# Optimization experiments

Measured on AMD Instinct MI355X. Metric: run time of the kernel, lower is better.

## Reference

```python
import jax, jax.numpy as jnp
import numpy as np

N, C, E, H = 100000, 128, 640000, 128


def setup_inputs() -> dict:
    key = jax.random.key(0)
    ks = jax.random.split(key, 8)
    x = jax.random.normal(ks[0], (N, C), dtype=jnp.float32)
    # edges guaranteed to have no self-loops (module removes them then re-adds clean self-loops)
    rol = jax.random.randint(ks[1], (E,), 0, N, dtype=jnp.int32)
    off = jax.random.randint(ks[2], (E,), 1, N, dtype=jnp.int32)
    col = (rol + off) % N
    edge_index = jnp.stack([rol, col])  # [2, E]
    s = 1.0 / np.sqrt(C)
    return {
        "x": x,
        "edge_index": edge_index,
        "W_emb": jax.random.normal(ks[3], (C, C), dtype=jnp.float32) * s,
        "b_emb": jnp.zeros((C,), dtype=jnp.float32),
        "Wa1": jax.random.normal(ks[4], (C, H), dtype=jnp.float32) * s,
        "ba1": jnp.zeros((H,), dtype=jnp.float32),
        "Wa2": jax.random.normal(ks[5], (H, 1), dtype=jnp.float32) * (1.0 / np.sqrt(H)),
        "ba2": jnp.zeros((1,), dtype=jnp.float32),
        "W_upd": jax.random.normal(ks[6], (C, C), dtype=jnp.float32) * s,
        "b_upd": jnp.zeros((C,), dtype=jnp.float32),
    }


def reference(x, edge_index, W_emb, b_emb, Wa1, ba1, Wa2, ba2, W_upd, b_upd):
    n = x.shape[0]
    loops = jnp.arange(n, dtype=edge_index.dtype)
    rol = jnp.concatenate([edge_index[0], loops])  # [E+N]
    col = jnp.concatenate([edge_index[1], loops])

    embedded_x = x @ W_emb + b_emb                     # [N, C]
    diff = x[rol] - x[col]                             # [E+N, C]
    h = jax.nn.leaky_relu(diff @ Wa1 + ba1, 0.01)      # [E+N, H]
    a = h @ Wa2 + ba2                                  # [E+N, 1]

    # segment softmax over incoming edges of each target node (col)
    amax = jax.ops.segment_max(a, col, num_segments=n)     # [N, 1]
    ea = jnp.exp(a - amax[col])
    denom = jax.ops.segment_sum(ea, col, num_segments=n)   # [N, 1]
    w = ea / (denom[col] + 1e-16)                           # [E+N, 1]

    msg = jax.ops.segment_sum(embedded_x[rol] * w, col, num_segments=n)  # [N, C]
    return msg @ W_upd + b_upd
```

## Files before the change

kernel.cpp:

```cpp
#include <hip/hip_runtime.h>
#include <hip/hip_bf16.h>

#define LRELU(t) ((t) > 0.0f ? (t) : 0.01f * (t))

typedef __attribute__((ext_vector_type(8))) short bf16x8;
typedef __attribute__((ext_vector_type(4))) float f32x4;

__device__ __forceinline__ unsigned short f2bf(float f) {
  unsigned u = __float_as_uint(f);
  u += 0x7fff + ((u >> 16) & 1);
  return (unsigned short)(u >> 16);
}
__device__ __forceinline__ float bflo(unsigned u) { return __uint_as_float(u << 16); }
__device__ __forceinline__ float bfhi(unsigned u) { return __uint_as_float(u & 0xffff0000u); }

__global__ __launch_bounds__(256) void wtrans_kernel(
    const float* __restrict__ W_emb, const float* __restrict__ Wa1,
    const float* __restrict__ W_upd, unsigned short* __restrict__ WtA,
    unsigned short* __restrict__ WtU) {
  int i = blockIdx.x * 256 + threadIdx.x;
  if (i < 32768) {
    int n = i >> 7, k = i & 127;
    float v = (n < 128) ? W_emb[k * 128 + n] : Wa1[k * 128 + (n - 128)];
    WtA[i] = f2bf(v);
  } else if (i < 49152) {
    int j = i - 32768;
    int n = j >> 7, k = j & 127;
    WtU[j] = f2bf(W_upd[k * 128 + n]);
  }
}

__global__ __launch_bounds__(256) void gemm_embP_kernel(
    const float* __restrict__ A, const unsigned short* __restrict__ Wt,
    const float* __restrict__ b_emb, unsigned short* __restrict__ C, int M) {
  const int lane = threadIdx.x & 63;
  const int w = threadIdx.x >> 6;
  const int row0 = blockIdx.x * 64;
  const int ncol0 = w * 64;
  const int lr = lane & 15;
  const int lg = lane >> 4;
  f32x4 acc[4][4];
#pragma unroll
  for (int mf = 0; mf < 4; ++mf)
#pragma unroll
    for (int nf = 0; nf < 4; ++nf) acc[mf][nf] = (f32x4){0.f, 0.f, 0.f, 0.f};

#pragma unroll
  for (int ks = 0; ks < 4; ++ks) {
    const int k0 = ks * 32 + lg * 8;
    bf16x8 bfr[4];
#pragma unroll
    for (int nf = 0; nf < 4; ++nf)
      bfr[nf] = *reinterpret_cast<const bf16x8*>(Wt + (size_t)(ncol0 + nf * 16 + lr) * 128 + k0);
    bf16x8 afr[4];
#pragma unroll
    for (int mf = 0; mf < 4; ++mf) {
      int row = row0 + mf * 16 + lr;
      if (row >= M) row = M - 1;
      const float* ap = A + (size_t)row * 128 + k0;
      float4 a0 = *reinterpret_cast<const float4*>(ap);
      float4 a1 = *reinterpret_cast<const float4*>(ap + 4);
      bf16x8 t;
      t[0] = (short)f2bf(a0.x); t[1] = (short)f2bf(a0.y);
      t[2] = (short)f2bf(a0.z); t[3] = (short)f2bf(a0.w);
      t[4] = (short)f2bf(a1.x); t[5] = (short)f2bf(a1.y);
      t[6] = (short)f2bf(a1.z); t[7] = (short)f2bf(a1.w);
      afr[mf] = t;
    }
#pragma unroll
    for (int mf = 0; mf < 4; ++mf)
#pragma unroll
      for (int nf = 0; nf < 4; ++nf)
        acc[mf][nf] =
            __builtin_amdgcn_mfma_f32_16x16x32_bf16(afr[mf], bfr[nf], acc[mf][nf], 0, 0, 0);
  }
#pragma unroll
  for (int nf = 0; nf < 4; ++nf) {
    int col = ncol0 + nf * 16 + lr;
    float bv = (col < 128) ? b_emb[col] : 0.0f;
#pragma unroll
    for (int mf = 0; mf < 4; ++mf) {
      int rowb = row0 + mf * 16 + lg * 4;
#pragma unroll
      for (int r = 0; r < 4; ++r) {
        int row = rowb + r;
        if (row < M) C[(size_t)row * 256 + col] = f2bf(acc[mf][nf][r] + bv);
      }
    }
  }
}

__global__ __launch_bounds__(256) void gemm_out_kernel(
    const unsigned short* __restrict__ Ab, const unsigned short* __restrict__ Wt,
    const float* __restrict__ b_upd, float* __restrict__ Cout, int M) {
  const int lane = threadIdx.x & 63;
  const int w = threadIdx.x >> 6;
  const int row0 = blockIdx.x * 128 + (w >> 1) * 64;
  const int ncol0 = (w & 1) * 64;
  const int lr = lane & 15;
  const int lg = lane >> 4;
  f32x4 acc[4][4];
#pragma unroll
  for (int mf = 0; mf < 4; ++mf)
#pragma unroll
    for (int nf = 0; nf < 4; ++nf) acc[mf][nf] = (f32x4){0.f, 0.f, 0.f, 0.f};

#pragma unroll
  for (int ks = 0; ks < 4; ++ks) {
    const int k0 = ks * 32 + lg * 8;
    bf16x8 bfr[4];
#pragma unroll
    for (int nf = 0; nf < 4; ++nf)
      bfr[nf] = *reinterpret_cast<const bf16x8*>(Wt + (size_t)(ncol0 + nf * 16 + lr) * 128 + k0);
    bf16x8 afr[4];
#pragma unroll
    for (int mf = 0; mf < 4; ++mf) {
      int row = row0 + mf * 16 + lr;
      if (row >= M) row = M - 1;
      afr[mf] = *reinterpret_cast<const bf16x8*>(Ab + (size_t)row * 128 + k0);
    }
#pragma unroll
    for (int mf = 0; mf < 4; ++mf)
#pragma unroll
      for (int nf = 0; nf < 4; ++nf)
        acc[mf][nf] =
            __builtin_amdgcn_mfma_f32_16x16x32_bf16(afr[mf], bfr[nf], acc[mf][nf], 0, 0, 0);
  }
#pragma unroll
  for (int nf = 0; nf < 4; ++nf) {
    int col = ncol0 + nf * 16 + lr;
    float bv = b_upd[col];
#pragma unroll
    for (int mf = 0; mf < 4; ++mf) {
      int rowb = row0 + mf * 16 + lg * 4;
#pragma unroll
      for (int r = 0; r < 4; ++r) {
        int row = rowb + r;
        if (row < M) Cout[(size_t)row * 128 + col] = acc[mf][nf][r] + bv;
      }
    }
  }
}

__global__ void zero_kernel(int* __restrict__ p, int n) {
  int i = blockIdx.x * blockDim.x + threadIdx.x;
  if (i < n) p[i] = 0;
}

__global__ void count_kernel(const int* __restrict__ col, int* __restrict__ counts, int E) {
  int e = blockIdx.x * blockDim.x + threadIdx.x;
  if (e < E) atomicAdd(&counts[col[e]], 1);
}

__global__ __launch_bounds__(1024) void scan1_kernel(const int* __restrict__ counts,
                                                     int* __restrict__ offsets,
                                                     int* __restrict__ bsum, int N, int N1) {
  __shared__ int sh[1024];
  int tid = threadIdx.x;
  int i = blockIdx.x * 1024 + tid;
  int v = (i < N) ? counts[i] : 0;
  sh[tid] = v;
  __syncthreads();
  for (int off = 1; off < 1024; off <<= 1) {
    int tv = (tid >= off) ? sh[tid - off] : 0;
    __syncthreads();
    sh[tid] += tv;
    __syncthreads();
  }
  if (i < N1) offsets[i] = sh[tid] - v;
  if (tid == 1023) bsum[blockIdx.x] = sh[1023];
}

__global__ __launch_bounds__(128) void scan2_kernel(int* __restrict__ bsum, int NB) {
  __shared__ int sh[128];
  int tid = threadIdx.x;
  int v = (tid < NB) ? bsum[tid] : 0;
  sh[tid] = v;
  __syncthreads();
  for (int off = 1; off < 128; off <<= 1) {
    int tv = (tid >= off) ? sh[tid - off] : 0;
    __syncthreads();
    sh[tid] += tv;
    __syncthreads();
  }
  if (tid < NB) bsum[tid] = sh[tid] - v;
}

__global__ __launch_bounds__(1024) void scan3_kernel(int* __restrict__ offsets,
                                                     const int* __restrict__ bsum,
                                                     int* __restrict__ cursor, int N, int N1) {
  int i = blockIdx.x * 1024 + threadIdx.x;
  if (i < N1) {
    int o = offsets[i] + bsum[blockIdx.x];
    offsets[i] = o;
    if (i < N) cursor[i] = o;
  }
}

__global__ __launch_bounds__(64) void prep_kernel(const float* __restrict__ ba1,
                                                  const float* __restrict__ Wa2,
                                                  const float* __restrict__ ba2,
                                                  float* __restrict__ a_self) {
  int l = threadIdx.x;
  float t1 = ba1[l], t2 = ba1[l + 64];
  float v = LRELU(t1) * Wa2[l] + LRELU(t2) * Wa2[l + 64];
#pragma unroll
  for (int off = 32; off > 0; off >>= 1) v += __shfl_xor(v, off);
  if (l == 0) *a_self = v + ba2[0];
}

__global__ void scatter_kernel(const int* __restrict__ rol, const int* __restrict__ col,
                               int* __restrict__ cursor, int* __restrict__ csr_rol, int E) {
  int e = blockIdx.x * blockDim.x + threadIdx.x;
  if (e < E) {
    int pos = atomicAdd(&cursor[col[e]], 1);
    csr_rol[pos] = rol[e];
  }
}

__global__ __launch_bounds__(256) void fused_kernel(
    const int* __restrict__ offsets, const int* __restrict__ csr_rol,
    const unsigned* __restrict__ embP, const float2* __restrict__ ba1_2,
    const float2* __restrict__ Wa2_2, const float* __restrict__ ba2,
    const float* __restrict__ a_self_p, unsigned* __restrict__ msgb, int N, int nwt) {
  const int lane = threadIdx.x & 63;
  const int wid = blockIdx.x * (blockDim.x >> 6) + (threadIdx.x >> 6);
  const float2 b2 = ba1_2[lane];
  const float2 w2 = Wa2_2[lane];
  const float ba2v = *ba2;
  const float aself = *a_self_p;

#define LOGIT(pp) (LRELU(bflo(pp) - pcx + b2.x) * w2.x + LRELU(bfhi(pp) - pcy + b2.y) * w2.y)
#define ONLINE(aval, ue)                      \
  {                                           \
    float nm = fmaxf(m, (aval));              \
    float cc = __expf(m - nm);                \
    float w = __expf((aval)-nm);              \
    s = s * cc + w;                           \
    ax = ax * cc + w * bflo(ue);              \
    ay = ay * cc + w * bfhi(ue);              \
    m = nm;                                   \
  }

  for (int n = wid; n < N; n += nwt) {
    int j0 = offsets[n], j1 = offsets[n + 1];
    unsigned ue_own = embP[(size_t)n * 128 + lane];
    unsigned up_own = embP[(size_t)n * 128 + 64 + lane];
    float pcx = bflo(up_own), pcy = bfhi(up_own);
    float m = aself, s = 1.0f;
    float ax = bflo(ue_own), ay = bfhi(ue_own);
    int j = j0;
    for (; j + 4 <= j1; j += 4) {
      int r0 = csr_rol[j], r1 = csr_rol[j + 1], r2 = csr_rol[j + 2], r3 = csr_rol[j + 3];
      unsigned pe0 = embP[(size_t)r0 * 128 + lane];
      unsigned pp0 = embP[(size_t)r0 * 128 + 64 + lane];
      unsigned pe1 = embP[(size_t)r1 * 128 + lane];
      unsigned pp1 = embP[(size_t)r1 * 128 + 64 + lane];
      unsigned pe2 = embP[(size_t)r2 * 128 + lane];
      unsigned pp2 = embP[(size_t)r2 * 128 + 64 + lane];
      unsigned pe3 = embP[(size_t)r3 * 128 + lane];
      unsigned pp3 = embP[(size_t)r3 * 128 + 64 + lane];
      float v0 = LOGIT(pp0), v1 = LOGIT(pp1), v2 = LOGIT(pp2), v3 = LOGIT(pp3);
#pragma unroll
      for (int off = 32; off > 0; off >>= 1) {
        v0 += __shfl_xor(v0, off);
        v1 += __shfl_xor(v1, off);
        v2 += __shfl_xor(v2, off);
        v3 += __shfl_xor(v3, off);
      }
      ONLINE(v0 + ba2v, pe0);
      ONLINE(v1 + ba2v, pe1);
      ONLINE(v2 + ba2v, pe2);
      ONLINE(v3 + ba2v, pe3);
    }
    for (; j < j1; ++j) {
      int r = csr_rol[j];
      unsigned pe = embP[(size_t)r * 128 + lane];
      unsigned pp = embP[(size_t)r * 128 + 64 + lane];
      float v = LOGIT(pp);
#pragma unroll
      for (int off = 32; off > 0; off >>= 1) v += __shfl_xor(v, off);
      ONLINE(v + ba2v, pe);
    }
    float inv = 1.0f / (s + 1e-16f);
    msgb[(size_t)n * 64 + lane] =
        (unsigned)f2bf(ax * inv) | ((unsigned)f2bf(ay * inv) << 16);
  }
#undef LOGIT
#undef ONLINE
}

extern "C" void kernel_launch(void* const* d_in, const int* in_sizes, int n_in,
                              void* d_out, int out_size, void* d_ws, size_t ws_size,
                              hipStream_t stream) {
  const float* x     = (const float*)d_in[0];
  const int*   ei    = (const int*)d_in[1];
  const float* W_emb = (const float*)d_in[2];
  const float* b_emb = (const float*)d_in[3];
  const float* Wa1   = (const float*)d_in[4];
  const float* ba1   = (const float*)d_in[5];
  const float* Wa2   = (const float*)d_in[6];
  const float* ba2   = (const float*)d_in[7];
  const float* W_upd = (const float*)d_in[8];
  const float* b_upd = (const float*)d_in[9];
  float* out = (float*)d_out;

  const int N = in_sizes[0] / 128;
  const int E = in_sizes[1] / 2;
  const int* rol = ei;
  const int* col = ei + E;

  char* base = (char*)d_ws;
  size_t off = 0;
  auto carve = [&](size_t bytes) {
    void* p = base + off;
    off = (off + bytes + 255) & ~(size_t)255;
    return p;
  };
  unsigned* embP   = (unsigned*)carve((size_t)N * 128 * 4);
  unsigned* msgb   = (unsigned*)carve((size_t)N * 64 * 4);
  unsigned short* WtA = (unsigned short*)carve(256 * 128 * 2);
  unsigned short* WtU = (unsigned short*)carve(128 * 128 * 2);
  int*      csr_rol= (int*)carve((size_t)E * 4);
  float*    a_self = (float*)carve(16);
  int*      counts = (int*)carve((size_t)N * 4);
  int*      offsets= (int*)carve((size_t)(N + 1) * 4);
  int*      cursor = (int*)carve((size_t)N * 4);
  int*      bsum   = (int*)carve(128 * 4);
  (void)ws_size;

  const int N1 = N + 1;
  const int NB = (N1 + 1023) / 1024;
  const int SBLK = 2048;
  const int NWT = SBLK * 4;

  zero_kernel<<<(N + 255) / 256, 256, 0, stream>>>(counts, N);
  wtrans_kernel<<<192, 256, 0, stream>>>(W_emb, Wa1, W_upd, WtA, WtU);

  gemm_embP_kernel<<<(N + 63) / 64, 256, 0, stream>>>(x, WtA, b_emb, (unsigned short*)embP, N);

  count_kernel<<<(E + 255) / 256, 256, 0, stream>>>(col, counts, E);
  scan1_kernel<<<NB, 1024, 0, stream>>>(counts, offsets, bsum, N, N1);
  scan2_kernel<<<1, 128, 0, stream>>>(bsum, NB);
  scan3_kernel<<<NB, 1024, 0, stream>>>(offsets, bsum, cursor, N, N1);
  prep_kernel<<<1, 64, 0, stream>>>(ba1, Wa2, ba2, a_self);
  scatter_kernel<<<(E + 255) / 256, 256, 0, stream>>>(rol, col, cursor, csr_rol, E);

  fused_kernel<<<SBLK, 256, 0, stream>>>(offsets, csr_rol, embP, (const float2*)ba1,
                                         (const float2*)Wa2, ba2, a_self, msgb, N, NWT);

  gemm_out_kernel<<<(N + 127) / 128, 256, 0, stream>>>((const unsigned short*)msgb, WtU, b_upd,
                                                       out, N);
}
```

Baseline: 346.4 us.

## Split attention logit across quarter-waves with permuted embedding layout and batched softmax

The embedding GEMM now stores each output row in a permuted, packed layout. This lets the fused edge kernel have each 16-lane quarter-wave compute the attention logit for one of four edges from a 16-byte vector load, instead of every lane loading and reducing each edge's full projection. The online softmax handles four edges per step with a single rescale and uses exp2 with log2e folded into Wa2. ba2 is dropped because it cancels in the softmax. W_upd rows are permuted to match the new message ordering. The aim is fewer cross-lane reduction shuffles and fewer exp calls per edge, at the cost of index-permutation complexity and some padded lanes on the tail iteration.

New measurement: 350.1 us. No clear change (+1.1%).

```diff
diff --git a/kernel.cpp b/kernel.cpp
--- a/kernel.cpp
+++ b/kernel.cpp
@@ -2,6 +2,7 @@
 #include <hip/hip_bf16.h>
 
 #define LRELU(t) ((t) > 0.0f ? (t) : 0.01f * (t))
+#define LOG2E 1.4426950408889634f
 
 typedef __attribute__((ext_vector_type(8))) short bf16x8;
 typedef __attribute__((ext_vector_type(4))) float f32x4;
@@ -13,6 +14,10 @@
 }
 __device__ __forceinline__ float bflo(unsigned u) { return __uint_as_float(u << 16); }
 __device__ __forceinline__ float bfhi(unsigned u) { return __uint_as_float(u & 0xffff0000u); }
+
+__device__ __forceinline__ int pilo(int s) {
+  return ((s >> 5) << 6) + ((s & 1) << 5) + ((s >> 1) & 15);
+}
 
 __global__ __launch_bounds__(256) void wtrans_kernel(
     const float* __restrict__ W_emb, const float* __restrict__ Wa1,
@@ -25,14 +30,16 @@
     WtA[i] = f2bf(v);
   } else if (i < 49152) {
     int j = i - 32768;
-    int n = j >> 7, k = j & 127;
-    WtU[j] = f2bf(W_upd[k * 128 + n]);
+    int n = j >> 7, k_st = j & 127;
+    int s = k_st >> 1;
+    int L = pilo(s) + ((k_st & 1) << 4);
+    WtU[j] = f2bf(W_upd[L * 128 + n]);
   }
 }
 
 __global__ __launch_bounds__(256) void gemm_embP_kernel(
     const float* __restrict__ A, const unsigned short* __restrict__ Wt,
-    const float* __restrict__ b_emb, unsigned short* __restrict__ C, int M) {
+    const float* __restrict__ b_emb, unsigned* __restrict__ embP, int M) {
   const int lane = threadIdx.x & 63;
   const int w = threadIdx.x >> 6;
   const int row0 = blockIdx.x * 64;
@@ -74,17 +81,27 @@
         acc[mf][nf] =
             __builtin_amdgcn_mfma_f32_16x16x32_bf16(afr[mf], bfr[nf], acc[mf][nf], 0, 0, 0);
   }
-#pragma unroll
-  for (int nf = 0; nf < 4; ++nf) {
-    int col = ncol0 + nf * 16 + lr;
-    float bv = (col < 128) ? b_emb[col] : 0.0f;
-#pragma unroll
-    for (int mf = 0; mf < 4; ++mf) {
-      int rowb = row0 + mf * 16 + lg * 4;
-#pragma unroll
-      for (int r = 0; r < 4; ++r) {
-        int row = rowb + r;
-        if (row < M) C[(size_t)row * 256 + col] = f2bf(acc[mf][nf][r] + bv);
+  float blo[2] = {0.f, 0.f}, bhi[2] = {0.f, 0.f};
+  if (ncol0 < 128) {
+#pragma unroll
+    for (int ph = 0; ph < 2; ++ph) {
+      int lo = ncol0 + 32 * ph + lr;
+      blo[ph] = b_emb[lo];
+      bhi[ph] = b_emb[lo + 16];
+    }
+  }
+#pragma unroll
+  for (int mf = 0; mf < 4; ++mf) {
+#pragma unroll
+    for (int r = 0; r < 4; ++r) {
+      int row = row0 + mf * 16 + lg * 4 + r;
+      if (row < M) {
+        unsigned w0 = (unsigned)f2bf(acc[mf][0][r] + blo[0]) |
+                      ((unsigned)f2bf(acc[mf][1][r] + bhi[0]) << 16);
+        unsigned w1 = (unsigned)f2bf(acc[mf][2][r] + blo[1]) |
+                      ((unsigned)f2bf(acc[mf][3][r] + bhi[1]) << 16);
+        *reinterpret_cast<uint2*>(embP + (size_t)row * 128 + w * 32 + lr * 2) =
+            make_uint2(w0, w1);
       }
     }
   }
@@ -199,14 +216,18 @@
 
 __global__ __launch_bounds__(64) void prep_kernel(const float* __restrict__ ba1,
                                                   const float* __restrict__ Wa2,
-                                                  const float* __restrict__ ba2,
-                                                  float* __restrict__ a_self) {
+                                                  float* __restrict__ a_self,
+                                                  float2* __restrict__ ba1p,
+                                                  float2* __restrict__ wa2p) {
   int l = threadIdx.x;
+  int d = pilo(l);
+  ba1p[l] = make_float2(ba1[d], ba1[d + 16]);
+  wa2p[l] = make_float2(Wa2[d] * LOG2E, Wa2[d + 16] * LOG2E);
   float t1 = ba1[l], t2 = ba1[l + 64];
   float v = LRELU(t1) * Wa2[l] + LRELU(t2) * Wa2[l + 64];
 #pragma unroll
   for (int off = 32; off > 0; off >>= 1) v += __shfl_xor(v, off);
-  if (l == 0) *a_self = v + ba2[0];
+  if (l == 0) *a_self = v * LOG2E;
 }
 
 __global__ void scatter_kernel(const int* __restrict__ rol, const int* __restrict__ col,
@@ -220,74 +241,74 @@
 
 __global__ __launch_bounds__(256) void fused_kernel(
     const int* __restrict__ offsets, const int* __restrict__ csr_rol,
-    const unsigned* __restrict__ embP, const float2* __restrict__ ba1_2,
-    const float2* __restrict__ Wa2_2, const float* __restrict__ ba2,
-    const float* __restrict__ a_self_p, unsigned* __restrict__ msgb, int N, int nwt) {
+    const unsigned* __restrict__ embP, const float2* __restrict__ ba1p,
+    const float2* __restrict__ wa2p, const float* __restrict__ a_self_p,
+    unsigned* __restrict__ msgb, int N, int nwt) {
   const int lane = threadIdx.x & 63;
+  const int q = lane & 15;
   const int wid = blockIdx.x * (blockDim.x >> 6) + (threadIdx.x >> 6);
-  const float2 b2 = ba1_2[lane];
-  const float2 w2 = Wa2_2[lane];
-  const float ba2v = *ba2;
+  const int g = lane >> 4;
+  float2 w4[4], b4[4];
+#pragma unroll
+  for (int k = 0; k < 4; ++k) {
+    w4[k] = wa2p[q * 4 + k];
+    b4[k] = ba1p[q * 4 + k];
+  }
   const float aself = *a_self_p;
-
-#define LOGIT(pp) (LRELU(bflo(pp) - pcx + b2.x) * w2.x + LRELU(bfhi(pp) - pcy + b2.y) * w2.y)
-#define ONLINE(aval, ue)                      \
-  {                                           \
-    float nm = fmaxf(m, (aval));              \
-    float cc = __expf(m - nm);                \
-    float w = __expf((aval)-nm);              \
-    s = s * cc + w;                           \
-    ax = ax * cc + w * bflo(ue);              \
-    ay = ay * cc + w * bfhi(ue);              \
-    m = nm;                                   \
-  }
 
   for (int n = wid; n < N; n += nwt) {
     int j0 = offsets[n], j1 = offsets[n + 1];
-    unsigned ue_own = embP[(size_t)n * 128 + lane];
-    unsigned up_own = embP[(size_t)n * 128 + 64 + lane];
-    float pcx = bflo(up_own), pcy = bfhi(up_own);
+    const unsigned* rowp = embP + (size_t)n * 128;
+    unsigned ue = rowp[lane];
+    uint4 pc4 = *reinterpret_cast<const uint4*>(rowp + 64 + q * 4);
+    float pm0 = bflo(pc4.x) - b4[0].x, pm1 = bfhi(pc4.x) - b4[0].y;
+    float pm2 = bflo(pc4.y) - b4[1].x, pm3 = bfhi(pc4.y) - b4[1].y;
+    float pm4 = bflo(pc4.z) - b4[2].x, pm5 = bfhi(pc4.z) - b4[2].y;
+    float pm6 = bflo(pc4.w) - b4[3].x, pm7 = bfhi(pc4.w) - b4[3].y;
     float m = aself, s = 1.0f;
-    float ax = bflo(ue_own), ay = bfhi(ue_own);
-    int j = j0;
-    for (; j + 4 <= j1; j += 4) {
-      int r0 = csr_rol[j], r1 = csr_rol[j + 1], r2 = csr_rol[j + 2], r3 = csr_rol[j + 3];
+    float ax = bflo(ue), ay = bfhi(ue);
+
+    for (int j = j0; j < j1; j += 4) {
+      int jj = j + g;
+      int jc = (jj < j1) ? jj : (j1 - 1);
+      int r = csr_rol[jc];
+      int r0 = __shfl(r, 0), r1 = __shfl(r, 16), r2 = __shfl(r, 32), r3 = __shfl(r, 48);
       unsigned pe0 = embP[(size_t)r0 * 128 + lane];
-      unsigned pp0 = embP[(size_t)r0 * 128 + 64 + lane];
       unsigned pe1 = embP[(size_t)r1 * 128 + lane];
-      unsigned pp1 = embP[(size_t)r1 * 128 + 64 + lane];
       unsigned pe2 = embP[(size_t)r2 * 128 + lane];
-      unsigned pp2 = embP[(size_t)r2 * 128 + 64 + lane];
       unsigned pe3 = embP[(size_t)r3 * 128 + lane];
-      unsigned pp3 = embP[(size_t)r3 * 128 + 64 + lane];
-      float v0 = LOGIT(pp0), v1 = LOGIT(pp1), v2 = LOGIT(pp2), v3 = LOGIT(pp3);
-#pragma unroll
-      for (int off = 32; off > 0; off >>= 1) {
-        v0 += __shfl_xor(v0, off);
-        v1 += __shfl_xor(v1, off);
-        v2 += __shfl_xor(v2, off);
-        v3 += __shfl_xor(v3, off);
-      }
-      ONLINE(v0 + ba2v, pe0);
-      ONLINE(v1 + ba2v, pe1);
-      ONLINE(v2 + ba2v, pe2);
-      ONLINE(v3 + ba2v, pe3);
-    }
-    for (; j < j1; ++j) {
-      int r = csr_rol[j];
-      unsigned pe = embP[(size_t)r * 128 + lane];
-      unsigned pp = embP[(size_t)r * 128 + 64 + lane];
-      float v = LOGIT(pp);
-#pragma unroll
-      for (int off = 32; off > 0; off >>= 1) v += __shfl_xor(v, off);
-      ONLINE(v + ba2v, pe);
-    }
-    float inv = 1.0f / (s + 1e-16f);
+      uint4 pp4 = *reinterpret_cast<const uint4*>(embP + (size_t)r * 128 + 64 + q * 4);
+      float t, v;
+      t = bflo(pp4.x) - pm0; t = fmaxf(t, 0.01f * t); v = t * w4[0].x;
+      t = bfhi(pp4.x) - pm1; t = fmaxf(t, 0.01f * t); v += t * w4[0].y;
+      t = bflo(pp4.y) - pm2; t = fmaxf(t, 0.01f * t); v += t * w4[1].x;
+      t = bfhi(pp4.y) - pm3; t = fmaxf(t, 0.01f * t); v += t * w4[1].y;
+      t = bflo(pp4.z) - pm4; t = fmaxf(t, 0.01f * t); v += t * w4[2].x;
+      t = bfhi(pp4.z) - pm5; t = fmaxf(t, 0.01f * t); v += t * w4[2].y;
+      t = bflo(pp4.w) - pm6; t = fmaxf(t, 0.01f * t); v += t * w4[3].x;
+      t = bfhi(pp4.w) - pm7; t = fmaxf(t, 0.01f * t); v += t * w4[3].y;
+      v += __shfl_xor(v, 1);
+      v += __shfl_xor(v, 2);
+      v += __shfl_xor(v, 4);
+      v += __shfl_xor(v, 8);
+      float v0 = __shfl(v, 0);
+      float s1 = __shfl(v, 16), s2 = __shfl(v, 32), s3 = __shfl(v, 48);
+      float v1 = (j + 1 < j1) ? s1 : -1e30f;
+      float v2 = (j + 2 < j1) ? s2 : -1e30f;
+      float v3 = (j + 3 < j1) ? s3 : -1e30f;
+      float nm = fmaxf(fmaxf(m, fmaxf(v0, v1)), fmaxf(v2, v3));
+      float cc = __builtin_exp2f(m - nm);
+      float e0 = __builtin_exp2f(v0 - nm), e1 = __builtin_exp2f(v1 - nm);
+      float e2 = __builtin_exp2f(v2 - nm), e3 = __builtin_exp2f(v3 - nm);
+      s = s * cc + ((e0 + e1) + (e2 + e3));
+      ax = ax * cc + ((e0 * bflo(pe0) + e1 * bflo(pe1)) + (e2 * bflo(pe2) + e3 * bflo(pe3)));
+      ay = ay * cc + ((e0 * bfhi(pe0) + e1 * bfhi(pe1)) + (e2 * bfhi(pe2) + e3 * bfhi(pe3)));
+      m = nm;
+    }
+    float inv = 1.0f / s;
     msgb[(size_t)n * 64 + lane] =
         (unsigned)f2bf(ax * inv) | ((unsigned)f2bf(ay * inv) << 16);
   }
-#undef LOGIT
-#undef ONLINE
 }
 
 extern "C" void kernel_launch(void* const* d_in, const int* in_sizes, int n_in,
@@ -300,7 +321,6 @@
   const float* Wa1   = (const float*)d_in[4];
   const float* ba1   = (const float*)d_in[5];
   const float* Wa2   = (const float*)d_in[6];
-  const float* ba2   = (const float*)d_in[7];
   const float* W_upd = (const float*)d_in[8];
   const float* b_upd = (const float*)d_in[9];
   float* out = (float*)d_out;
@@ -321,6 +341,8 @@
   unsigned* msgb   = (unsigned*)carve((size_t)N * 64 * 4);
   unsigned short* WtA = (unsigned short*)carve(256 * 128 * 2);
   unsigned short* WtU = (unsigned short*)carve(128 * 128 * 2);
+  float2*   ba1p   = (float2*)carve(64 * 8);
+  float2*   wa2p   = (float2*)carve(64 * 8);
   int*      csr_rol= (int*)carve((size_t)E * 4);
   float*    a_self = (float*)carve(16);
   int*      counts = (int*)carve((size_t)N * 4);
@@ -337,17 +359,17 @@
   zero_kernel<<<(N + 255) / 256, 256, 0, stream>>>(counts, N);
   wtrans_kernel<<<192, 256, 0, stream>>>(W_emb, Wa1, W_upd, WtA, WtU);
 
-  gemm_embP_kernel<<<(N + 63) / 64, 256, 0, stream>>>(x, WtA, b_emb, (unsigned short*)embP, N);
+  gemm_embP_kernel<<<(N + 63) / 64, 256, 0, stream>>>(x, WtA, b_emb, embP, N);
 
   count_kernel<<<(E + 255) / 256, 256, 0, stream>>>(col, counts, E);
   scan1_kernel<<<NB, 1024, 0, stream>>>(counts, offsets, bsum, N, N1);
   scan2_kernel<<<1, 128, 0, stream>>>(bsum, NB);
   scan3_kernel<<<NB, 1024, 0, stream>>>(offsets, bsum, cursor, N, N1);
-  prep_kernel<<<1, 64, 0, stream>>>(ba1, Wa2, ba2, a_self);
+  prep_kernel<<<1, 64, 0, stream>>>(ba1, Wa2, a_self, ba1p, wa2p);
   scatter_kernel<<<(E + 255) / 256, 256, 0, stream>>>(rol, col, cursor, csr_rol, E);
 
-  fused_kernel<<<SBLK, 256, 0, stream>>>(offsets, csr_rol, embP, (const float2*)ba1,
-                                         (const float2*)Wa2, ba2, a_self, msgb, N, NWT);
+  fused_kernel<<<SBLK, 256, 0, stream>>>(offsets, csr_rol, embP, ba1p, wa2p, a_self, msgb, N,
+                                         NWT);
 
   gemm_out_kernel<<<(N + 127) / 128, 256, 0, stream>>>((const unsigned short*)msgb, WtU, b_upd,
                                                        out, N);
```
